# Performance work log

Measured on AMD Instinct MI355X. Metric: run time of the kernel, lower is better.

## Reference

```python
import jax, jax.numpy as jnp
import numpy as np

F = 128          # num_features
NRBF = 20        # num_rbf_features
N_NODES = 25000
N_EDGES = 400000


def setup_inputs() -> dict:
    key = jax.random.key(0)
    ks = jax.random.split(key, 12)
    inp = {
        "idx_i": jax.random.randint(ks[0], (N_EDGES,), 0, N_NODES, dtype=jnp.int32),
        "idx_j": jax.random.randint(ks[1], (N_EDGES,), 0, N_NODES, dtype=jnp.int32),
        "rel_dir": jax.random.normal(ks[2], (N_EDGES, 3), dtype=jnp.float32),
        "rel_dist_cut": jax.random.uniform(ks[3], (N_EDGES,), dtype=jnp.float32),
        "rbf_features": jax.random.normal(ks[4], (N_EDGES, NRBF), dtype=jnp.float32),
        "scalar_features": jax.random.normal(ks[5], (N_NODES, F), dtype=jnp.float32),
        "vector_features": jax.random.normal(ks[6], (N_NODES, F, 3), dtype=jnp.float32),
        # scalar_network: Linear(F,F) -> SiLU -> Linear(F,3F)
        "W1": jax.random.normal(ks[7], (F, F), dtype=jnp.float32) / np.sqrt(F),
        "b1": jnp.zeros((F,), dtype=jnp.float32),
        "W2": jax.random.normal(ks[8], (3 * F, F), dtype=jnp.float32) / np.sqrt(F),
        "b2": jnp.zeros((3 * F,), dtype=jnp.float32),
        # rbf_network: Linear(NRBF, 3F)
        "Wr": jax.random.normal(ks[9], (3 * F, NRBF), dtype=jnp.float32) / np.sqrt(NRBF),
        "br": jnp.zeros((3 * F,), dtype=jnp.float32),
    }
    return inp


def reference(idx_i, idx_j, rel_dir, rel_dist_cut, rbf_features,
              scalar_features, vector_features, W1, b1, W2, b2, Wr, br):
    n_nodes = scalar_features.shape[0]
    # phi: per-node MLP -> [N, 3F]
    h = jax.nn.silu(scalar_features @ W1.T + b1)
    phi = h @ W2.T + b2
    # W: RBF-derived edge weights gated by cosine-cut distance -> [E, 3F]
    W = (rbf_features @ Wr.T + br) * rel_dist_cut[:, None]
    phi_W = phi[idx_j] * W                                  # [E, 3F]
    phi_W_vv, phi_W_ss, phi_W_vs = jnp.split(phi_W, 3, axis=-1)
    # scatter-add scalar residuals
    scalar_res = jax.ops.segment_sum(phi_W_ss, idx_i, num_segments=n_nodes)
    # per-edge vector messages [E, F, 3]
    vec_per_edge = (vector_features[idx_j] * phi_W_vv[..., None]
                    + phi_W_vs[..., None] * rel_dir[:, None, :])
    vector_res = jax.ops.segment_sum(vec_per_edge, idx_i, num_segments=n_nodes)
    return scalar_features + scalar_res, vector_features + vector_res
```

## Files before the change

### kernel.cpp

```cpp
#include <hip/hip_runtime.h>
#include <hip/hip_fp16.h>

#define F 128
#define F3 384
#define NRBF 20
#define NPB 16
#define CHUNK 64

typedef unsigned int u32;
typedef _Float16 half8 __attribute__((ext_vector_type(8)));
typedef float floatx4 __attribute__((ext_vector_type(4)));

__device__ __forceinline__ float2 uph(u32 u) {
    __half2 h = *(__half2*)&u;
    return __half22float2(h);
}
__device__ __forceinline__ u32 pkh(float a, float b) {
    __half2 h = __floats2half2_rn(a, b);
    return *(u32*)&h;
}

__device__ __forceinline__ float fdot2f(u32 a, u32 b, float c) {
#if defined(__has_builtin)
#if __has_builtin(__builtin_amdgcn_fdot2)
    typedef _Float16 h2 __attribute__((ext_vector_type(2)));
    return __builtin_amdgcn_fdot2(*(h2*)&a, *(h2*)&b, c, false);
#else
    float2 fa = uph(a), fb = uph(b);
    return fmaf(fa.x, fb.x, fmaf(fa.y, fb.y, c));
#endif
#else
    float2 fa = uph(a), fb = uph(b);
    return fmaf(fa.x, fb.x, fmaf(fa.y, fb.y, c));
#endif
}

__global__ void prep_kernel(const float* __restrict__ Wr,
                            const float* __restrict__ W1, const float* __restrict__ W2,
                            u32* __restrict__ WrTh, _Float16* __restrict__ Wh,
                            int* __restrict__ counts, int n_nodes) {
    int t = blockIdx.x * blockDim.x + threadIdx.x;
    if (t < 10 * F3) {
        int rr = t / F3, f = t % F3;
        WrTh[rr * F3 + f] = pkh(Wr[f * NRBF + 2 * rr], Wr[f * NRBF + 2 * rr + 1]);
        return;
    }
    int u = t - 10 * F3;
    if (u < (F + F3) * F) {
        int n = u >> 7, k = u & (F - 1);
        float w = (n < F) ? W1[n * F + k] : W2[(size_t)(n - F) * F + k];
        Wh[u] = (_Float16)w;
        return;
    }
    int z = u - (F + F3) * F;
    if (z < n_nodes) counts[z] = 0;
}

__global__ void hist_kernel(const int* __restrict__ idx_i, int* __restrict__ counts, int n_edges) {
    int e = blockIdx.x * blockDim.x + threadIdx.x;
    if (e < n_edges) atomicAdd(&counts[idx_i[e]], 1);
}

#define SCAN_T 1024
#define SCAN_MAXN 25600
__launch_bounds__(SCAN_T)
__global__ void scan_lds_kernel(const int* __restrict__ counts, int* __restrict__ row_start,
                                int* __restrict__ cursor, int n) {
    __shared__ int sbuf[SCAN_MAXN];
    __shared__ int partial[SCAN_T];
    int t = threadIdx.x;
    for (int i = t; i < n; i += SCAN_T) sbuf[i] = counts[i];
    __syncthreads();
    int C = (n + SCAN_T - 1) / SCAN_T;
    int beg = t * C, end = min(beg + C, n);
    int sum = 0;
    for (int i = beg; i < end; i++) sum += sbuf[i];
    partial[t] = sum;
    __syncthreads();
    for (int off = 1; off < SCAN_T; off <<= 1) {
        int v = (t >= off) ? partial[t - off] : 0;
        __syncthreads();
        partial[t] += v;
        __syncthreads();
    }
    int base = (t == 0) ? 0 : partial[t - 1];
    for (int i = beg; i < end; i++) { int c = sbuf[i]; sbuf[i] = base; base += c; }
    __syncthreads();
    for (int i = t; i < n; i += SCAN_T) { int v = sbuf[i]; row_start[i] = v; cursor[i] = v; }
    if (t == SCAN_T - 1) row_start[n] = partial[SCAN_T - 1];
}

__launch_bounds__(1024)
__global__ void scan_kernel(const int* __restrict__ counts, int* __restrict__ row_start,
                            int* __restrict__ cursor, int n) {
    __shared__ int partial[1024];
    int t = threadIdx.x;
    int C = (n + 1023) / 1024;
    int beg = t * C, end = min(beg + C, n);
    int sum = 0;
    for (int i = beg; i < end; i++) sum += counts[i];
    partial[t] = sum;
    __syncthreads();
    for (int off = 1; off < 1024; off <<= 1) {
        int v = (t >= off) ? partial[t - off] : 0;
        __syncthreads();
        partial[t] += v;
        __syncthreads();
    }
    int base = (t == 0) ? 0 : partial[t - 1];
    for (int i = beg; i < end; i++) {
        int c = counts[i];
        row_start[i] = base; cursor[i] = base; base += c;
    }
    if (t == 1023) row_start[n] = partial[1023];
}

__launch_bounds__(256)
__global__ void fusedD_kernel(const float* __restrict__ sf,
                              const _Float16* __restrict__ Wh,
                              const float* __restrict__ b1, const float* __restrict__ b2,
                              const float* __restrict__ vf, __half* __restrict__ gbufh,
                              const int* __restrict__ idx_i, const int* __restrict__ idx_j,
                              const float* __restrict__ rel_dir, const float* __restrict__ rdc,
                              const float* __restrict__ rbf,
                              int* __restrict__ cursor, u32* __restrict__ recs,
                              int n_nodes, int n_edges, int PHB) {
    __shared__ _Float16 hl[4][16][136];
    int blk = blockIdx.x, tid = threadIdx.x;

    if (blk >= PHB) {
        int e = (blk - PHB) * 256 + tid;
        if (e >= n_edges) return;
        int p = atomicAdd(&cursor[idx_i[e]], 1);
        u32 r[16];
        r[0] = (u32)idx_j[e];
        r[1] = __float_as_uint(rdc[e]);
        r[2] = __float_as_uint(rel_dir[e * 3 + 0]);
        r[3] = __float_as_uint(rel_dir[e * 3 + 1]);
        r[4] = __float_as_uint(rel_dir[e * 3 + 2]);
        const float* rb = rbf + (size_t)e * NRBF;
#pragma unroll
        for (int t = 0; t < 10; t++) r[5 + t] = pkh(rb[2 * t], rb[2 * t + 1]);
        r[15] = 0;
        float4* dst = (float4*)(recs + (size_t)p * 16);
        const float4* src = (const float4*)r;
        dst[0] = src[0]; dst[1] = src[1]; dst[2] = src[2]; dst[3] = src[3];
        return;
    }

    int lane = tid & 63;
    int wv = tid >> 6;
    int col = lane & 15;
    int kg = lane >> 4;
    int row0 = blk * 64 + wv * 16;

    half8 a1[4];
#pragma unroll
    for (int kb = 0; kb < 4; kb++) {
        int rr = row0 + col;
        if (rr >= n_nodes) rr = n_nodes - 1;
        const float4* xp = (const float4*)(sf + (size_t)rr * F + kb * 32 + kg * 8);
        float4 x0 = xp[0], x1 = xp[1];
        half8 a;
        a[0] = (_Float16)x0.x; a[1] = (_Float16)x0.y; a[2] = (_Float16)x0.z; a[3] = (_Float16)x0.w;
        a[4] = (_Float16)x1.x; a[5] = (_Float16)x1.y; a[6] = (_Float16)x1.z; a[7] = (_Float16)x1.w;
        a1[kb] = a;
    }

    floatx4 acc[8];
#pragma unroll
    for (int nt = 0; nt < 8; nt++) acc[nt] = (floatx4){0.f, 0.f, 0.f, 0.f};
#pragma unroll
    for (int nt = 0; nt < 8; nt++) {
#pragma unroll
        for (int kb = 0; kb < 4; kb++) {
            half8 b = *(const half8*)(Wh + (size_t)(nt * 16 + col) * F + kb * 32 + kg * 8);
            acc[nt] = __builtin_amdgcn_mfma_f32_16x16x32_f16(a1[kb], b, acc[nt], 0, 0, 0);
        }
    }
#pragma unroll
    for (int nt = 0; nt < 8; nt++) {
        int f1 = nt * 16 + col;
        float bb = b1[f1];
#pragma unroll
        for (int r = 0; r < 4; r++) {
            float v = acc[nt][r] + bb;
            float s = v / (1.f + __expf(-v));
            hl[wv][kg * 4 + r][f1] = (_Float16)s;
        }
    }

    half8 a2[4];
#pragma unroll
    for (int kb = 0; kb < 4; kb++)
        a2[kb] = *(const half8*)&hl[wv][col][kb * 32 + kg * 8];

#pragma unroll
    for (int c = 0; c < 3; c++) {
#pragma unroll
        for (int nt = 0; nt < 8; nt++) acc[nt] = (floatx4){0.f, 0.f, 0.f, 0.f};
#pragma unroll
        for (int nt = 0; nt < 8; nt++) {
#pragma unroll
            for (int kb = 0; kb < 4; kb++) {
                half8 b = *(const half8*)(Wh + (size_t)(F + c * 128 + nt * 16 + col) * F + kb * 32 + kg * 8);
                acc[nt] = __builtin_amdgcn_mfma_f32_16x16x32_f16(a2[kb], b, acc[nt], 0, 0, 0);
            }
        }
#pragma unroll
        for (int nt = 0; nt < 8; nt++) {
            int f2 = c * 128 + nt * 16 + col;
            float bb = b2[f2];
            int slot = (f2 & 63) * 12 + ((f2 >> 6) & 1) * 6 + (f2 >> 7);
#pragma unroll
            for (int r = 0; r < 4; r++) {
                int node = row0 + kg * 4 + r;
                if (node < n_nodes)
                    gbufh[(size_t)node * 768 + slot] = __float2half(acc[nt][r] + bb);
            }
        }
    }

    int base = blk * 64;
    for (int idx = tid; idx < 64 * 64; idx += 256) {
        int nl = idx >> 6, ln = idx & 63;
        int node = base + nl;
        if (node < n_nodes) {
            const float* v = vf + (size_t)node * F3;
            u32* gp = (u32*)(gbufh + (size_t)node * 768 + ln * 12);
            float a0 = v[ln * 3 + 0], a1v = v[ln * 3 + 1], a2v = v[ln * 3 + 2];
            float c0 = v[(ln + 64) * 3 + 0], c1 = v[(ln + 64) * 3 + 1], c2 = v[(ln + 64) * 3 + 2];
            ((__half*)gp)[3] = __float2half(a0);
            gp[2] = pkh(a1v, a2v);
            ((__half*)gp)[9] = __float2half(c0);
            gp[5] = pkh(c1, c2);
        }
    }
}

__global__ void scatter_kernel(const int* __restrict__ idx_i, int* __restrict__ cursor,
                               int* __restrict__ edge_order, int n_edges) {
    int e = blockIdx.x * blockDim.x + threadIdx.x;
    if (e < n_edges) {
        int p = atomicAdd(&cursor[idx_i[e]], 1);
        edge_order[p] = e;
    }
}

__launch_bounds__(256)
__global__ void gather5_kernel(const float* __restrict__ sf, const float* __restrict__ vf,
                               const u32* __restrict__ WrTh, const float* __restrict__ br,
                               const u32* __restrict__ gbuf, const u32* __restrict__ recs,
                               const int* __restrict__ row_start,
                               float* __restrict__ out_s, float* __restrict__ out_v,
                               int n_nodes) {
    __shared__ u32 lsm[4][CHUNK * 16];
    int tid = threadIdx.x;
    int lane = tid & 63;
    int wvid = tid >> 6;
    int w = wvid & 1;
    int node = blockIdx.x * 2 + (wvid >> 1);
    if (node >= n_nodes) return;
    u32* lds = lsm[wvid];

    int fb = lane + 64 * w;
    u32 wrpk[3][10];
    float brv[3];
#pragma unroll
    for (int k = 0; k < 3; k++) {
        brv[k] = br[fb + 128 * k];
#pragma unroll
        for (int rr = 0; rr < 10; rr++)
            wrpk[k][rr] = WrTh[rr * F3 + fb + 128 * k];
    }

    float acc_s = 0.f, av0 = 0.f, av1 = 0.f, av2 = 0.f;
    int beg = row_start[node];
    int end = row_start[node + 1];

    for (int cb = beg; cb < end; cb += CHUNK) {
        int cnt = min(CHUNK, end - cb);
        {
            const float4* src = (const float4*)(recs + (size_t)cb * 16);
            int nf4 = cnt * 4;
            for (int t = lane; t < nf4; t += 64)
                ((float4*)lds)[t] = src[t];
        }

        auto issueL = [&](u32& g0, u32& g1, u32& g2, int m) {
            if (m < cnt) {
                int j = (int)lds[m * 16];
                const u32* gp = gbuf + (size_t)j * 384 + lane * 6 + w * 3;
                g0 = gp[0]; g1 = gp[1]; g2 = gp[2];
            }
        };
        auto computeE = [&](u32 g0, u32 g1, u32 g2, int m) {
            const uint4* q = (const uint4*)(lds + m * 16);
            uint4 q0 = q[0], q1 = q[1], q2 = q[2], q3 = q[3];
            float rd = __uint_as_float(q0.y);
            float dx = __uint_as_float(q0.z);
            float dy = __uint_as_float(q0.w);
            float dz = __uint_as_float(q1.x);
            u32 rbu[10] = { q1.y, q1.z, q1.w, q2.x, q2.y, q2.z, q2.w, q3.x, q3.y, q3.z };
            float W0 = brv[0], W1f = brv[1], W2f = brv[2];
#pragma unroll
            for (int rr = 0; rr < 10; rr++) {
                W0  = fdot2f(rbu[rr], wrpk[0][rr], W0);
                W1f = fdot2f(rbu[rr], wrpk[1][rr], W1f);
                W2f = fdot2f(rbu[rr], wrpk[2][rr], W2f);
            }
            float2 p01  = uph(g0);
            float2 p2v0 = uph(g1);
            float2 v12  = uph(g2);
            float pw0 = W0  * rd * p01.x;
            float pw1 = W1f * rd * p01.y;
            float pw2 = W2f * rd * p2v0.x;
            acc_s += pw1;
            av0 += p2v0.y * pw0 + pw2 * dx;
            av1 += v12.x  * pw0 + pw2 * dy;
            av2 += v12.y  * pw0 + pw2 * dz;
        };

        u32 A0, A1, A2, B0, B1, B2, C0, C1, C2, D0, D1, D2;
        issueL(A0, A1, A2, 0); issueL(B0, B1, B2, 1);
        issueL(C0, C1, C2, 2); issueL(D0, D1, D2, 3);
        int m = 0;
        while (true) {
            if (m >= cnt) break; computeE(A0, A1, A2, m); m++; issueL(A0, A1, A2, m + 3);
            if (m >= cnt) break; computeE(B0, B1, B2, m); m++; issueL(B0, B1, B2, m + 3);
            if (m >= cnt) break; computeE(C0, C1, C2, m); m++; issueL(C0, C1, C2, m + 3);
            if (m >= cnt) break; computeE(D0, D1, D2, m); m++; issueL(D0, D1, D2, m + 3);
        }
    }

    out_s[(size_t)node * F + fb] = sf[(size_t)node * F + fb] + acc_s;
    const float* vfi = vf + (size_t)node * F3 + fb * 3;
    float* ovi = out_v + (size_t)node * F3 + fb * 3;
    ovi[0] = vfi[0] + av0;
    ovi[1] = vfi[1] + av1;
    ovi[2] = vfi[2] + av2;
}

__launch_bounds__(256)
__global__ void gather3_kernel(const int* __restrict__ idx_j,
                               const float* __restrict__ rel_dir, const float* __restrict__ rdc,
                               const float* __restrict__ rbf,
                               const float* __restrict__ sf, const float* __restrict__ vf,
                               const u32* __restrict__ WrTh, const float* __restrict__ br,
                               const u32* __restrict__ gbuf,
                               const int* __restrict__ row_start, const int* __restrict__ edge_order,
                               float* __restrict__ out_s, float* __restrict__ out_v,
                               int n_nodes) {
    int lane = threadIdx.x & 63;
    int w = (threadIdx.x >> 6) & 1;
    int node = blockIdx.x * 2 + (threadIdx.x >> 7);
    if (node >= n_nodes) return;

    int fb = lane + 64 * w;
    u32 wrpk[3][10];
    float brv[3];
#pragma unroll
    for (int k = 0; k < 3; k++) {
        brv[k] = br[fb + 128 * k];
#pragma unroll
        for (int rr = 0; rr < 10; rr++)
            wrpk[k][rr] = WrTh[rr * F3 + fb + 128 * k];
    }

    float acc_s = 0.f, av0 = 0.f, av1 = 0.f, av2 = 0.f;
    int beg = row_start[node];
    int end = row_start[node + 1];

    for (int cb = beg; cb < end; cb += 64) {
        int cnt = min(64, end - cb);
        int jv = 0; float rdv = 0.f, dxv = 0.f, dyv = 0.f, dzv = 0.f;
        u32 rbm[10];
#pragma unroll
        for (int rr = 0; rr < 10; rr++) rbm[rr] = 0;
        if (lane < cnt) {
            int e = edge_order[cb + lane];
            jv = idx_j[e];
            rdv = rdc[e];
            dxv = rel_dir[e * 3 + 0]; dyv = rel_dir[e * 3 + 1]; dzv = rel_dir[e * 3 + 2];
            const float4* rp = (const float4*)(rbf + (size_t)e * NRBF);
            float4 r0 = rp[0], r1 = rp[1], r2 = rp[2], r3 = rp[3], r4 = rp[4];
            rbm[0] = pkh(r0.x, r0.y); rbm[1] = pkh(r0.z, r0.w);
            rbm[2] = pkh(r1.x, r1.y); rbm[3] = pkh(r1.z, r1.w);
            rbm[4] = pkh(r2.x, r2.y); rbm[5] = pkh(r2.z, r2.w);
            rbm[6] = pkh(r3.x, r3.y); rbm[7] = pkh(r3.z, r3.w);
            rbm[8] = pkh(r4.x, r4.y); rbm[9] = pkh(r4.z, r4.w);
        }
        auto issue = [&](u32& g0, u32& g1, u32& g2, int k) {
            int j = __shfl(jv, k, 64);
            const u32* gp = gbuf + (size_t)j * 384 + lane * 6 + w * 3;
            g0 = gp[0]; g1 = gp[1]; g2 = gp[2];
        };
        auto compute = [&](u32 g0, u32 g1, u32 g2, int k) {
            float rd = __shfl(rdv, k, 64);
            float dx = __shfl(dxv, k, 64);
            float dy = __shfl(dyv, k, 64);
            float dz = __shfl(dzv, k, 64);
            float W0 = brv[0], W1f = brv[1], W2f = brv[2];
#pragma unroll
            for (int rr = 0; rr < 10; rr++) {
                u32 rbi = (u32)__shfl((int)rbm[rr], k, 64);
                W0  = fdot2f(rbi, wrpk[0][rr], W0);
                W1f = fdot2f(rbi, wrpk[1][rr], W1f);
                W2f = fdot2f(rbi, wrpk[2][rr], W2f);
            }
            float2 p01 = uph(g0);
            float2 p2v0 = uph(g1);
            float2 v12 = uph(g2);
            float pw0 = W0 * rd * p01.x;
            float pw1 = W1f * rd * p01.y;
            float pw2 = W2f * rd * p2v0.x;
            acc_s += pw1;
            av0 += p2v0.y * pw0 + pw2 * dx;
            av1 += v12.x  * pw0 + pw2 * dy;
            av2 += v12.y  * pw0 + pw2 * dz;
        };
        u32 A0, A1, A2, B0, B1, B2;
        issue(A0, A1, A2, 0);
        int k = 0;
        while (k + 2 <= cnt) {
            issue(B0, B1, B2, k + 1);
            compute(A0, A1, A2, k);
            if (k + 2 < cnt) issue(A0, A1, A2, k + 2);
            compute(B0, B1, B2, k + 1);
            k += 2;
        }
        if (k < cnt) compute(A0, A1, A2, k);
    }

    out_s[(size_t)node * F + fb] = sf[(size_t)node * F + fb] + acc_s;
    const float* vfi = vf + (size_t)node * F3 + fb * 3;
    float* ovi = out_v + (size_t)node * F3 + fb * 3;
    ovi[0] = vfi[0] + av0;
    ovi[1] = vfi[1] + av1;
    ovi[2] = vfi[2] + av2;
}

__global__ void transpose_wr(const float* __restrict__ Wr, float* __restrict__ WrT) {
    int idx = blockIdx.x * blockDim.x + threadIdx.x;
    if (idx < F3 * NRBF) {
        int f = idx / NRBF, r = idx % NRBF;
        WrT[r * F3 + f] = Wr[idx];
    }
}

__global__ void init_out(const float* __restrict__ sf, const float* __restrict__ vf,
                         float* __restrict__ out, int n_scalar, int n_total) {
    int i = blockIdx.x * blockDim.x + threadIdx.x;
    int n4 = n_total >> 2;
    if (i < n4) {
        float4 v;
        int base = i << 2;
        if (base < n_scalar) v = ((const float4*)sf)[i];
        else                 v = ((const float4*)vf)[i - (n_scalar >> 2)];
        ((float4*)out)[i] = v;
    }
}

__launch_bounds__(256)
__global__ void phi32_kernel(const float* __restrict__ sf,
                             const float* __restrict__ W1, const float* __restrict__ b1,
                             const float* __restrict__ W2, const float* __restrict__ b2,
                             float* __restrict__ phi, int n_nodes) {
    __shared__ float xs[NPB][F];
    __shared__ float hs[NPB][F];
    int tid = threadIdx.x;
    int nb = blockIdx.x * NPB;
    for (int t = tid; t < NPB * F / 4; t += 256) {
        int n  = t / (F / 4);
        int k4 = t % (F / 4);
        float4 v = make_float4(0.f, 0.f, 0.f, 0.f);
        if (nb + n < n_nodes) v = ((const float4*)(sf + (size_t)(nb + n) * F))[k4];
        ((float4*)&xs[n][0])[k4] = v;
    }
    __syncthreads();
    {
        int f = tid & (F - 1);
        int half_ = tid >> 7;
        float acc[8];
#pragma unroll
        for (int nn = 0; nn < 8; nn++) acc[nn] = 0.f;
        const float* w1row = W1 + (size_t)f * F;
        for (int k = 0; k < F; k++) {
            float w = w1row[k];
#pragma unroll
            for (int nn = 0; nn < 8; nn++)
                acc[nn] += xs[half_ * 8 + nn][k] * w;
        }
        float b = b1[f];
#pragma unroll
        for (int nn = 0; nn < 8; nn++) {
            float v = acc[nn] + b;
            hs[half_ * 8 + nn][f] = v / (1.f + __expf(-v));
        }
    }
    __syncthreads();
    for (int f = tid; f < F3; f += 256) {
        float acc[NPB];
#pragma unroll
        for (int n = 0; n < NPB; n++) acc[n] = 0.f;
        const float* w2row = W2 + (size_t)f * F;
        for (int k = 0; k < F; k++) {
            float w = w2row[k];
#pragma unroll
            for (int n = 0; n < NPB; n++)
                acc[n] += hs[n][k] * w;
        }
        float b = b2[f];
        for (int n = 0; n < NPB; n++)
            if (nb + n < n_nodes)
                phi[(size_t)(nb + n) * F3 + f] = acc[n] + b;
    }
}

__launch_bounds__(256)
__global__ void edge_kernel(const int* __restrict__ idx_i, const int* __restrict__ idx_j,
                            const float* __restrict__ rel_dir, const float* __restrict__ rdc,
                            const float* __restrict__ rbf,
                            const float* __restrict__ vf,
                            const float* __restrict__ WrT, const float* __restrict__ br,
                            const float* __restrict__ phi,
                            float* __restrict__ out_s, float* __restrict__ out_v,
                            int n_edges) {
    int lane = threadIdx.x & 63;
    int e = (int)((blockIdx.x * (unsigned)blockDim.x + threadIdx.x) >> 6);
    if (e >= n_edges) return;
    int i = idx_i[e], j = idx_j[e];
    float rd = rdc[e];
    float d0 = rel_dir[e * 3 + 0], d1 = rel_dir[e * 3 + 1], d2 = rel_dir[e * 3 + 2];
    float rb[NRBF];
#pragma unroll
    for (int r = 0; r < NRBF; r++) rb[r] = rbf[(size_t)e * NRBF + r];
    const float* pj = phi + (size_t)j * F3;
    float pw[6];
#pragma unroll
    for (int q = 0; q < 6; q++) {
        int f = lane + 64 * q;
        float acc = br[f];
#pragma unroll
        for (int r = 0; r < NRBF; r++)
            acc += rb[r] * WrT[r * F3 + f];
        pw[q] = acc * rd * pj[f];
    }
    atomicAdd(&out_s[(size_t)i * F + lane],       pw[2]);
    atomicAdd(&out_s[(size_t)i * F + lane + 64],  pw[3]);
    const float* vfj = vf + (size_t)j * F * 3;
    float* ovi = out_v + (size_t)i * F * 3;
#pragma unroll
    for (int h = 0; h < 2; h++) {
        int f = lane + 64 * h;
        float vv = pw[h];
        float vs = pw[4 + h];
        atomicAdd(&ovi[f * 3 + 0], vfj[f * 3 + 0] * vv + vs * d0);
        atomicAdd(&ovi[f * 3 + 1], vfj[f * 3 + 1] * vv + vs * d1);
        atomicAdd(&ovi[f * 3 + 2], vfj[f * 3 + 2] * vv + vs * d2);
    }
}

extern "C" void kernel_launch(void* const* d_in, const int* in_sizes, int n_in,
                              void* d_out, int out_size, void* d_ws, size_t ws_size,
                              hipStream_t stream) {
    const int*   idx_i   = (const int*)d_in[0];
    const int*   idx_j   = (const int*)d_in[1];
    const float* rel_dir = (const float*)d_in[2];
    const float* rdc     = (const float*)d_in[3];
    const float* rbf     = (const float*)d_in[4];
    const float* sf      = (const float*)d_in[5];
    const float* vf      = (const float*)d_in[6];
    const float* W1      = (const float*)d_in[7];
    const float* b1      = (const float*)d_in[8];
    const float* W2      = (const float*)d_in[9];
    const float* b2      = (const float*)d_in[10];
    const float* Wr      = (const float*)d_in[11];
    const float* br      = (const float*)d_in[12];

    int E = in_sizes[0];
    int N = in_sizes[5] / F;

    float* out_s = (float*)d_out;
    float* out_v = out_s + (size_t)N * F;

    size_t off = 0;
    auto slab = [&](size_t bytes) { size_t o = off; off = (off + bytes + 255) & ~(size_t)255; return o; };
    size_t o_wrth = slab((size_t)10 * F3 * sizeof(u32));
    size_t o_wh   = slab((size_t)(F + F3) * F * sizeof(_Float16));
    size_t o_gbuf = slab((size_t)N * 768 * sizeof(__half));
    size_t o_cnt  = slab((size_t)N * sizeof(int));
    size_t o_row  = slab((size_t)(N + 1) * sizeof(int));
    size_t o_rec  = slab((size_t)E * 64);
    size_t need_v5 = off;

    size_t off3 = 0;
    auto slab3 = [&](size_t bytes) { size_t o = off3; off3 = (off3 + bytes + 255) & ~(size_t)255; return o; };
    size_t t_wrth = slab3((size_t)10 * F3 * sizeof(u32));
    size_t t_wh   = slab3((size_t)(F + F3) * F * sizeof(_Float16));
    size_t t_gbuf = slab3((size_t)N * 768 * sizeof(__half));
    size_t t_cnt  = slab3((size_t)N * sizeof(int));
    size_t t_row  = slab3((size_t)(N + 1) * sizeof(int));
    size_t t_ord  = slab3((size_t)E * sizeof(int));
    size_t need_v3 = off3;

    int prep_threads = 10 * F3 + (F + F3) * F + N;
    int HB = (E + 255) / 256;
    int PHB = (N + 63) / 64;

    if (ws_size >= need_v5) {
        u32*      WrTh      = (u32*)((char*)d_ws + o_wrth);
        _Float16* Wh        = (_Float16*)((char*)d_ws + o_wh);
        __half*   gbufh     = (__half*)((char*)d_ws + o_gbuf);
        u32*      gbuf      = (u32*)gbufh;
        int*      counts    = (int*)((char*)d_ws + o_cnt);
        int*      cursor    = counts;
        int*      row_start = (int*)((char*)d_ws + o_row);
        u32*      recs      = (u32*)((char*)d_ws + o_rec);

        prep_kernel<<<(prep_threads + 255) / 256, 256, 0, stream>>>(Wr, W1, W2, WrTh, Wh, counts, N);
        hist_kernel<<<HB, 256, 0, stream>>>(idx_i, counts, E);
        if (N <= SCAN_MAXN)
            scan_lds_kernel<<<1, SCAN_T, 0, stream>>>(counts, row_start, cursor, N);
        else
            scan_kernel<<<1, 1024, 0, stream>>>(counts, row_start, cursor, N);
        fusedD_kernel<<<PHB + HB, 256, 0, stream>>>(sf, Wh, b1, b2, vf, gbufh,
                                                    idx_i, idx_j, rel_dir, rdc, rbf,
                                                    cursor, recs, N, E, PHB);
        gather5_kernel<<<(N + 1) / 2, 256, 0, stream>>>(sf, vf, WrTh, br, gbuf, recs,
                                                        row_start, out_s, out_v, N);
    } else if (ws_size >= need_v3) {
        u32*      WrTh      = (u32*)((char*)d_ws + t_wrth);
        _Float16* Wh        = (_Float16*)((char*)d_ws + t_wh);
        __half*   gbufh     = (__half*)((char*)d_ws + t_gbuf);
        u32*      gbuf      = (u32*)gbufh;
        int*      counts    = (int*)((char*)d_ws + t_cnt);
        int*      cursor    = counts;
        int*      row_start = (int*)((char*)d_ws + t_row);
        int*      edge_ord  = (int*)((char*)d_ws + t_ord);

        prep_kernel<<<(prep_threads + 255) / 256, 256, 0, stream>>>(Wr, W1, W2, WrTh, Wh, counts, N);
        hist_kernel<<<HB, 256, 0, stream>>>(idx_i, counts, E);
        if (N <= SCAN_MAXN)
            scan_lds_kernel<<<1, SCAN_T, 0, stream>>>(counts, row_start, cursor, N);
        else
            scan_kernel<<<1, 1024, 0, stream>>>(counts, row_start, cursor, N);
        fusedD_kernel<<<PHB, 256, 0, stream>>>(sf, Wh, b1, b2, vf, gbufh,
                                               idx_i, idx_j, rel_dir, rdc, rbf,
                                               cursor, nullptr, N, E, PHB);
        scatter_kernel<<<HB, 256, 0, stream>>>(idx_i, cursor, edge_ord, E);
        gather3_kernel<<<(N + 1) / 2, 256, 0, stream>>>(idx_j, rel_dir, rdc, rbf, sf, vf,
                                                        WrTh, br, gbuf, row_start, edge_ord,
                                                        out_s, out_v, N);
    } else {
        size_t off2 = 0;
        auto slab2 = [&](size_t bytes) { size_t o = off2; off2 = (off2 + bytes + 255) & ~(size_t)255; return o; };
        size_t f_wrt = slab2((size_t)F3 * NRBF * sizeof(float));
        size_t f_phi = slab2((size_t)N * F3 * sizeof(float));
        float* WrT = (float*)((char*)d_ws + f_wrt);
        float* phi = (float*)((char*)d_ws + f_phi);

        int n_scalar = N * F;
        int n_total  = N * F * 4;
        init_out<<<(n_total / 4 + 255) / 256, 256, 0, stream>>>(sf, vf, (float*)d_out, n_scalar, n_total);
        transpose_wr<<<(F3 * NRBF + 255) / 256, 256, 0, stream>>>(Wr, WrT);
        phi32_kernel<<<(N + NPB - 1) / NPB, 256, 0, stream>>>(sf, W1, b1, W2, b2, phi, N);
        edge_kernel<<<(E + 3) / 4, 256, 0, stream>>>(idx_i, idx_j, rel_dir, rdc, rbf,
                                                     vf, WrT, br, phi, out_s, out_v, E);
    }
}
```

Measured before the change: 228.3 us.

## Split fused phi/record kernel and stage phi output in LDS for coalesced stores

Splits the fused kernel that computed the per-node MLP and built the edge records into two separate launches. The phi kernel now writes its half-precision outputs and the vector features into an LDS staging buffer for 32 nodes per block, then copies them to global memory as contiguous 16-byte stores. Before, it wrote scattered 2-byte global stores. Each block also shrinks to 2 waves. The extra kernel launch loses the overlap between record building and the MLP, and the LDS staging adds block barriers.

```diff
diff --git a/kernel.cpp b/kernel.cpp
--- a/kernel.cpp
+++ b/kernel.cpp
@@ -6,6 +6,7 @@
 #define NRBF 20
 #define NPB 16
 #define CHUNK 64
+#define PSN 32
 
 typedef unsigned int u32;
 typedef _Float16 half8 __attribute__((ext_vector_type(8)));
@@ -115,44 +116,53 @@
     if (t == 1023) row_start[n] = partial[1023];
 }
 
-__launch_bounds__(256)
-__global__ void fusedD_kernel(const float* __restrict__ sf,
-                              const _Float16* __restrict__ Wh,
-                              const float* __restrict__ b1, const float* __restrict__ b2,
-                              const float* __restrict__ vf, __half* __restrict__ gbufh,
-                              const int* __restrict__ idx_i, const int* __restrict__ idx_j,
+__global__ void build_records(const int* __restrict__ idx_i, const int* __restrict__ idx_j,
                               const float* __restrict__ rel_dir, const float* __restrict__ rdc,
-                              const float* __restrict__ rbf,
-                              int* __restrict__ cursor, u32* __restrict__ recs,
-                              int n_nodes, int n_edges, int PHB) {
-    __shared__ _Float16 hl[4][16][136];
-    int blk = blockIdx.x, tid = threadIdx.x;
-
-    if (blk >= PHB) {
-        int e = (blk - PHB) * 256 + tid;
-        if (e >= n_edges) return;
+                              const float* __restrict__ rbf, int* __restrict__ cursor,
+                              u32* __restrict__ recs, int n_edges) {
+    int e = blockIdx.x * blockDim.x + threadIdx.x;
+    if (e >= n_edges) return;
+    int p = atomicAdd(&cursor[idx_i[e]], 1);
+    u32 r[16];
+    r[0] = (u32)idx_j[e];
+    r[1] = __float_as_uint(rdc[e]);
+    r[2] = __float_as_uint(rel_dir[e * 3 + 0]);
+    r[3] = __float_as_uint(rel_dir[e * 3 + 1]);
+    r[4] = __float_as_uint(rel_dir[e * 3 + 2]);
+    const float* rb = rbf + (size_t)e * NRBF;
+#pragma unroll
+    for (int t = 0; t < 10; t++) r[5 + t] = pkh(rb[2 * t], rb[2 * t + 1]);
+    r[15] = 0;
+    float4* dst = (float4*)(recs + (size_t)p * 16);
+    const float4* src = (const float4*)r;
+    dst[0] = src[0]; dst[1] = src[1]; dst[2] = src[2]; dst[3] = src[3];
+}
+
+__global__ void scatter_kernel(const int* __restrict__ idx_i, int* __restrict__ cursor,
+                               int* __restrict__ edge_order, int n_edges) {
+    int e = blockIdx.x * blockDim.x + threadIdx.x;
+    if (e < n_edges) {
         int p = atomicAdd(&cursor[idx_i[e]], 1);
-        u32 r[16];
-        r[0] = (u32)idx_j[e];
-        r[1] = __float_as_uint(rdc[e]);
-        r[2] = __float_as_uint(rel_dir[e * 3 + 0]);
-        r[3] = __float_as_uint(rel_dir[e * 3 + 1]);
-        r[4] = __float_as_uint(rel_dir[e * 3 + 2]);
-        const float* rb = rbf + (size_t)e * NRBF;
-#pragma unroll
-        for (int t = 0; t < 10; t++) r[5 + t] = pkh(rb[2 * t], rb[2 * t + 1]);
-        r[15] = 0;
-        float4* dst = (float4*)(recs + (size_t)p * 16);
-        const float4* src = (const float4*)r;
-        dst[0] = src[0]; dst[1] = src[1]; dst[2] = src[2]; dst[3] = src[3];
-        return;
-    }
-
+        edge_order[p] = e;
+    }
+}
+
+__launch_bounds__(128)
+__global__ void phi_stage_kernel(const float* __restrict__ sf,
+                                 const _Float16* __restrict__ Wh,
+                                 const float* __restrict__ b1, const float* __restrict__ b2,
+                                 const float* __restrict__ vf, __half* __restrict__ gbufh,
+                                 int n_nodes) {
+    __shared__ __align__(16) _Float16 stage[PSN * 768];
+    _Float16 (*hl)[16][136] = reinterpret_cast<_Float16 (*)[16][136]>(stage);
+
+    int tid = threadIdx.x;
     int lane = tid & 63;
     int wv = tid >> 6;
     int col = lane & 15;
     int kg = lane >> 4;
-    int row0 = blk * 64 + wv * 16;
+    int base = blockIdx.x * PSN;
+    int row0 = base + wv * 16;
 
     half8 a1[4];
 #pragma unroll
@@ -189,11 +199,13 @@
             hl[wv][kg * 4 + r][f1] = (_Float16)s;
         }
     }
+    __syncthreads();
 
     half8 a2[4];
 #pragma unroll
     for (int kb = 0; kb < 4; kb++)
         a2[kb] = *(const half8*)&hl[wv][col][kb * 32 + kg * 8];
+    __syncthreads();
 
 #pragma unroll
     for (int c = 0; c < 3; c++) {
@@ -214,36 +226,33 @@
             int slot = (f2 & 63) * 12 + ((f2 >> 6) & 1) * 6 + (f2 >> 7);
 #pragma unroll
             for (int r = 0; r < 4; r++) {
-                int node = row0 + kg * 4 + r;
-                if (node < n_nodes)
-                    gbufh[(size_t)node * 768 + slot] = __float2half(acc[nt][r] + bb);
+                int nl = wv * 16 + kg * 4 + r;
+                stage[nl * 768 + slot] = (_Float16)(acc[nt][r] + bb);
             }
         }
     }
 
-    int base = blk * 64;
-    for (int idx = tid; idx < 64 * 64; idx += 256) {
+    for (int idx = tid; idx < PSN * 64; idx += 128) {
         int nl = idx >> 6, ln = idx & 63;
         int node = base + nl;
         if (node < n_nodes) {
             const float* v = vf + (size_t)node * F3;
-            u32* gp = (u32*)(gbufh + (size_t)node * 768 + ln * 12);
-            float a0 = v[ln * 3 + 0], a1v = v[ln * 3 + 1], a2v = v[ln * 3 + 2];
-            float c0 = v[(ln + 64) * 3 + 0], c1 = v[(ln + 64) * 3 + 1], c2 = v[(ln + 64) * 3 + 2];
-            ((__half*)gp)[3] = __float2half(a0);
-            gp[2] = pkh(a1v, a2v);
-            ((__half*)gp)[9] = __float2half(c0);
-            gp[5] = pkh(c1, c2);
-        }
-    }
-}
-
-__global__ void scatter_kernel(const int* __restrict__ idx_i, int* __restrict__ cursor,
-                               int* __restrict__ edge_order, int n_edges) {
-    int e = blockIdx.x * blockDim.x + threadIdx.x;
-    if (e < n_edges) {
-        int p = atomicAdd(&cursor[idx_i[e]], 1);
-        edge_order[p] = e;
+            _Float16* s = stage + nl * 768 + ln * 12;
+            s[3]  = (_Float16)v[ln * 3 + 0];
+            s[4]  = (_Float16)v[ln * 3 + 1];
+            s[5]  = (_Float16)v[ln * 3 + 2];
+            s[9]  = (_Float16)v[(ln + 64) * 3 + 0];
+            s[10] = (_Float16)v[(ln + 64) * 3 + 1];
+            s[11] = (_Float16)v[(ln + 64) * 3 + 2];
+        }
+    }
+    __syncthreads();
+
+    const uint4* s4 = (const uint4*)stage;
+    uint4* g4 = (uint4*)gbufh + (size_t)base * 96;
+    for (int t = tid; t < PSN * 96; t += 128) {
+        int node = base + t / 96;
+        if (node < n_nodes) g4[t] = s4[t];
     }
 }
 
@@ -606,7 +615,7 @@
 
     int prep_threads = 10 * F3 + (F + F3) * F + N;
     int HB = (E + 255) / 256;
-    int PHB = (N + 63) / 64;
+    int PSB = (N + PSN - 1) / PSN;
 
     if (ws_size >= need_v5) {
         u32*      WrTh      = (u32*)((char*)d_ws + o_wrth);
@@ -624,9 +633,8 @@
             scan_lds_kernel<<<1, SCAN_T, 0, stream>>>(counts, row_start, cursor, N);
         else
             scan_kernel<<<1, 1024, 0, stream>>>(counts, row_start, cursor, N);
-        fusedD_kernel<<<PHB + HB, 256, 0, stream>>>(sf, Wh, b1, b2, vf, gbufh,
-                                                    idx_i, idx_j, rel_dir, rdc, rbf,
-                                                    cursor, recs, N, E, PHB);
+        build_records<<<HB, 256, 0, stream>>>(idx_i, idx_j, rel_dir, rdc, rbf, cursor, recs, E);
+        phi_stage_kernel<<<PSB, 128, 0, stream>>>(sf, Wh, b1, b2, vf, gbufh, N);
         gather5_kernel<<<(N + 1) / 2, 256, 0, stream>>>(sf, vf, WrTh, br, gbuf, recs,
                                                         row_start, out_s, out_v, N);
     } else if (ws_size >= need_v3) {
@@ -645,9 +653,7 @@
             scan_lds_kernel<<<1, SCAN_T, 0, stream>>>(counts, row_start, cursor, N);
         else
             scan_kernel<<<1, 1024, 0, stream>>>(counts, row_start, cursor, N);
-        fusedD_kernel<<<PHB, 256, 0, stream>>>(sf, Wh, b1, b2, vf, gbufh,
-                                               idx_i, idx_j, rel_dir, rdc, rbf,
-                                               cursor, nullptr, N, E, PHB);
+        phi_stage_kernel<<<PSB, 128, 0, stream>>>(sf, Wh, b1, b2, vf, gbufh, N);
         scatter_kernel<<<HB, 256, 0, stream>>>(idx_i, cursor, edge_ord, E);
         gather3_kernel<<<(N + 1) / 2, 256, 0, stream>>>(idx_j, rel_dir, rdc, rbf, sf, vf,
                                                         WrTh, br, gbuf, row_start, edge_ord,
```

Measured after the change: 220.9 us. -3.2%, faster.
